# Kernel optimization log

Measured on AMD Instinct MI355X. Metric: run time of the kernel, lower is better.

Reference implementation:

```python
import jax, jax.numpy as jnp
import numpy as np

TEMPERATURE = 0.07
HARD_NEG_RATIO = 0.5
B, D, N_CLASSES = 2048, 512, 100


def setup_inputs() -> dict:
    key = jax.random.key(0)
    kf, kl = jax.random.split(key)
    features = jax.random.normal(kf, (B, D), dtype=jnp.float32)
    # L2-normalize as is standard for SupCon embeddings (keeps logits well-scaled)
    features = features / jnp.linalg.norm(features, axis=1, keepdims=True)
    labels = jax.random.randint(kl, (B,), 0, N_CLASSES, dtype=jnp.int64)
    return {"features": features, "labels": labels}


def reference(features, labels):
    b = features.shape[0]
    dt = features.dtype
    lab = labels.reshape(-1, 1)
    mask = (lab == lab.T).astype(dt)                       # [B,B] positives (incl. self)
    adc = (features @ features.T) / TEMPERATURE            # [B,B] logits
    logits_max = jax.lax.stop_gradient(jnp.max(adc, axis=1, keepdims=True))
    logits = adc - logits_max                              # row-stabilized
    logits_mask = 1.0 - jnp.eye(b, dtype=dt)               # exclude self
    negative_mask = (1.0 - mask) * logits_mask
    neg_b = negative_mask > 0

    # top-k hard-negative threshold: k-th largest negative logit (global over all pairs).
    # k is data-dependent, so use a full descending sort + dynamic gather (jit-safe).
    flat = jnp.where(neg_b, logits, -jnp.inf).ravel()      # [B*B]
    sorted_desc = -jnp.sort(-flat)
    n_neg = jnp.sum(neg_b)
    k = jnp.maximum(1, (HARD_NEG_RATIO * n_neg).astype(jnp.int32))  # floor, >=1
    threshold = sorted_desc[k - 1]
    hard_negatives_mask = ((logits >= threshold) & neg_b).astype(dt)

    final_mask = jnp.minimum(mask + hard_negatives_mask, 1.0) * logits_mask
    row_pos = final_mask.sum(axis=1)
    single_samples = (row_pos == 0).astype(dt)

    exp_logits = jnp.exp(logits) * logits_mask
    log_prob = logits - jnp.log(exp_logits.sum(axis=1, keepdims=True) + 1e-12)
    mean_log_prob_pos = (final_mask * log_prob).sum(axis=1) / (row_pos + single_samples)
    loss_vec = -mean_log_prob_pos * (1.0 - single_samples)
    loss = loss_vec.sum() / (b - single_samples.sum())
    return (loss, hard_negatives_mask, final_mask)
```

## Files before the change

kernel.cpp:

```cpp
#include <hip/hip_runtime.h>
#include <cstddef>

constexpr int Bn   = 2048;
constexpr int Dn   = 512;
constexpr int NCLS = 100;
constexpr int CAP  = 131072;
constexpr unsigned WWIN = 32768;


struct Ctl {
  unsigned above;
  unsigned candCount;
  unsigned singles;
  unsigned done;
  float    thrF;
  unsigned pad1;
  double   lossSum;
  unsigned hist[4096];
  unsigned cand[CAP];
};
static_assert(offsetof(Ctl, cand) % 16 == 0, "cand must be 16B aligned");
static_assert(offsetof(Ctl, cand) == 16416, "zeroed head size");

__device__ inline unsigned key_of(float L) {
  unsigned u = __float_as_uint(L);
  return (u & 0x80000000u) ? ~u : (u | 0x80000000u);
}
__device__ inline float key_to_float(unsigned key) {
  unsigned u = (key & 0x80000000u) ? (key ^ 0x80000000u) : ~key;
  return __uint_as_float(u);
}
__device__ inline unsigned wlo_key() {
  const float c0 = -1.0f / 0.07f;
  return key_of(c0) - (WWIN / 2);
}
__device__ inline void store16_a4(float* p, float4 v) {
  __builtin_memcpy((void*)p, &v, 16);
}

__global__ __launch_bounds__(256) void rowdot_k(const float* __restrict__ F,
                                                float* __restrict__ rm, Ctl* c) {
  const int i = blockIdx.x * 256 + threadIdx.x;
  const float4* p = (const float4*)(F + (size_t)i * Dn);
  float acc = 0.0f;
#pragma unroll 16
  for (int q = 0; q < 128; ++q) {
    const float4 f = p[q];
    acc = __builtin_fmaf(f.x, f.x, acc);
    acc = __builtin_fmaf(f.y, f.y, acc);
    acc = __builtin_fmaf(f.z, f.z, acc);
    acc = __builtin_fmaf(f.w, f.w, acc);
  }
  rm[i] = acc / 0.07f;
  unsigned* cz = (unsigned*)c;
  for (int idx = i; idx < 4104; idx += 2048) cz[idx] = 0;
}

__global__ __launch_bounds__(256) void gemm_adc(const float* __restrict__ F,
                                                const float* __restrict__ rm,
                                                const int* __restrict__ labels,
                                                float* __restrict__ adc, Ctl* c) {
  __shared__ float smem[4352];
  __shared__ int slabi[64], slabj[64];
  __shared__ float rmiA[64], rmjA[64];
  __shared__ unsigned wlist[1024];
  __shared__ unsigned wcnt, abcnt, gbase;
  const int t = threadIdx.x;
  int r = 0;
  { const int idx = blockIdx.x; while ((r + 1) * (r + 2) / 2 <= idx) ++r; }
  const int cc = blockIdx.x - r * (r + 1) / 2;
  const int i0 = r * 64, j0 = cc * 64;

  const int tx = t & 15, ty = t >> 4;
  const int lrow = t >> 2, lq = t & 3;

  if (t < 64) {
    slabi[t] = labels[i0 + t]; rmiA[t] = rm[i0 + t];
    slabj[t] = labels[j0 + t]; rmjA[t] = rm[j0 + t];
  }
  if (t == 0) { wcnt = 0; abcnt = 0; gbase = 0; }

  float acc[4][4] = {};
  const float* Ab = F + (size_t)(i0 + lrow) * Dn;
  const float* Bb = F + (size_t)(j0 + lrow) * Dn;
  float* As = smem;
  float* Bs = smem + 2176;

  float4 a = *(const float4*)(Ab + lq * 4);
  float4 b = *(const float4*)(Bb + lq * 4);
  {
    const int k0 = lq * 4;
    As[(k0 + 0) * 68 + lrow] = a.x; As[(k0 + 1) * 68 + lrow] = a.y;
    As[(k0 + 2) * 68 + lrow] = a.z; As[(k0 + 3) * 68 + lrow] = a.w;
    Bs[(k0 + 0) * 68 + lrow] = b.x; Bs[(k0 + 1) * 68 + lrow] = b.y;
    Bs[(k0 + 2) * 68 + lrow] = b.z; Bs[(k0 + 3) * 68 + lrow] = b.w;
  }
  __syncthreads();

  for (int ch = 0; ch < 32; ++ch) {
    const int cur = ch & 1, nxt = cur ^ 1;
    if (ch < 31) {
      const int kg = (ch + 1) * 16;
      a = *(const float4*)(Ab + kg + lq * 4);
      b = *(const float4*)(Bb + kg + lq * 4);
    }
    const float* Ac = As + cur * 1088;
    const float* Bc = Bs + cur * 1088;
#pragma unroll
    for (int k = 0; k < 16; ++k) {
      const float4 av = *(const float4*)(Ac + k * 68 + ty * 4);
      const float4 bv = *(const float4*)(Bc + k * 68 + tx * 4);
      const float aa[4] = {av.x, av.y, av.z, av.w};
      const float bb[4] = {bv.x, bv.y, bv.z, bv.w};
#pragma unroll
      for (int m = 0; m < 4; ++m)
#pragma unroll
        for (int n = 0; n < 4; ++n)
          acc[m][n] = __builtin_fmaf(aa[m], bb[n], acc[m][n]);
    }
    if (ch < 31) {
      const int k0 = lq * 4;
      float* An = As + nxt * 1088;
      float* Bm = Bs + nxt * 1088;
      An[(k0 + 0) * 68 + lrow] = a.x; An[(k0 + 1) * 68 + lrow] = a.y;
      An[(k0 + 2) * 68 + lrow] = a.z; An[(k0 + 3) * 68 + lrow] = a.w;
      Bm[(k0 + 0) * 68 + lrow] = b.x; Bm[(k0 + 1) * 68 + lrow] = b.y;
      Bm[(k0 + 2) * 68 + lrow] = b.z; Bm[(k0 + 3) * 68 + lrow] = b.w;
    }
    __syncthreads();
  }

  float v[4][4];
#pragma unroll
  for (int m = 0; m < 4; ++m) {
#pragma unroll
    for (int n = 0; n < 4; ++n) v[m][n] = acc[m][n] / 0.07f;
    float4 q = {v[m][0], v[m][1], v[m][2], v[m][3]};
    *(float4*)&adc[(size_t)(i0 + ty * 4 + m) * Bn + j0 + tx * 4] = q;
  }
  if (r != cc) {
    __syncthreads();
    float* T = smem;
#pragma unroll
    for (int m = 0; m < 4; ++m)
#pragma unroll
      for (int n = 0; n < 4; ++n)
        T[(tx * 4 + n) * 68 + (ty * 4 + m)] = v[m][n];
    __syncthreads();
#pragma unroll
    for (int e = 0; e < 4; ++e) {
      const int row2 = e * 16 + ty;
      *(float4*)&adc[(size_t)(j0 + row2) * Bn + i0 + tx * 4] =
          *(const float4*)(T + row2 * 68 + tx * 4);
    }
  }

  __syncthreads();
  const unsigned klo = wlo_key(), khi = klo + WWIN;
  unsigned myab = 0;
#pragma unroll
  for (int m = 0; m < 4; ++m) {
    const int gi = i0 + ty * 4 + m;
    const int li = slabi[ty * 4 + m];
    const float rmi = rmiA[ty * 4 + m];
#pragma unroll
    for (int n = 0; n < 4; ++n) {
      const int gj = j0 + tx * 4 + n;
      if (gi == gj || li == slabj[tx * 4 + n]) continue;
      const unsigned key = key_of(v[m][n] - rmi);
      if (key >= khi) ++myab;
      else if (key >= klo) {
        atomicAdd(&c->hist[(key - klo) >> 3], 1u);
        const unsigned p = atomicAdd(&wcnt, 1u);
        if (p < 1024u) wlist[p] = key;
      }
      if (r != cc) {
        const unsigned key2 = key_of(v[m][n] - rmjA[tx * 4 + n]);
        if (key2 >= khi) ++myab;
        else if (key2 >= klo) {
          atomicAdd(&c->hist[(key2 - klo) >> 3], 1u);
          const unsigned p = atomicAdd(&wcnt, 1u);
          if (p < 1024u) wlist[p] = key2;
        }
      }
    }
  }
  if (myab) atomicAdd(&abcnt, myab);
  __syncthreads();
  if (t == 0) {
    if (abcnt) atomicAdd(&c->above, abcnt);
    const unsigned nl = wcnt < 1024u ? wcnt : 1024u;
    gbase = nl ? atomicAdd(&c->candCount, nl) : 0u;
  }
  __syncthreads();
  const unsigned nl = wcnt < 1024u ? wcnt : 1024u;
  for (unsigned q = t; q < nl; q += 256) {
    const unsigned p = gbase + q;
    if (p < (unsigned)CAP) c->cand[p] = wlist[q];
  }
}

__global__ __launch_bounds__(256) void select_k(const int* __restrict__ labels, Ctl* c) {
  __shared__ unsigned cnt[NCLS];
  __shared__ unsigned tsum[256], suffix[256];
  __shared__ unsigned skk;
  __shared__ int sbd;
  __shared__ unsigned sab, m;
  __shared__ unsigned list[256];
  const int t = threadIdx.x;
  if (t < NCLS) cnt[t] = 0;
  if (t == 0) { m = 0; sbd = 0; sab = 0; }
  __syncthreads();
  for (int j = t; j < Bn; j += 256) atomicAdd(&cnt[labels[j]], 1u);
  __syncthreads();
  if (t == 0) {
    unsigned s = 0;
    for (int h = 0; h < NCLS; ++h) s += cnt[h] * cnt[h];
    unsigned nneg = (unsigned)Bn * Bn - s;
    unsigned k = nneg >> 1;
    if (k < 1) k = 1;
    skk = k;
  }
  const uint4* hp = (const uint4*)c->hist;
  uint4 h0 = hp[t * 4 + 0], h1 = hp[t * 4 + 1], h2 = hp[t * 4 + 2], h3 = hp[t * 4 + 3];
  const unsigned hv[16] = {h0.x, h0.y, h0.z, h0.w, h1.x, h1.y, h1.z, h1.w,
                           h2.x, h2.y, h2.z, h2.w, h3.x, h3.y, h3.z, h3.w};
  unsigned s = 0;
#pragma unroll
  for (int u = 0; u < 16; ++u) s += hv[u];
  tsum[t] = s;
  __syncthreads();
  if (t == 0) {
    unsigned acc = c->above;
    for (int q = 255; q >= 0; --q) { suffix[q] = acc; acc += tsum[q]; }
  }
  __syncthreads();
  const unsigned kk = skk;
  unsigned cum = suffix[t];
#pragma unroll
  for (int u = 15; u >= 0; --u) {
    if (cum < kk && cum + hv[u] >= kk) { sbd = t * 16 + u; sab = cum; }
    cum += hv[u];
  }
  __syncthreads();
  const int bd = sbd;
  const unsigned rr = kk - sab;
  const unsigned klo = wlo_key();
  unsigned n = c->candCount; if (n > (unsigned)CAP) n = (unsigned)CAP;
  const unsigned n4 = n >> 2;
  const uint4* cp = (const uint4*)c->cand;
  unsigned q = t;
  for (; q + 7u * 256u < n4; q += 8u * 256u) {
    uint4 v[8];
#pragma unroll
    for (int u = 0; u < 8; ++u) v[u] = cp[q + (unsigned)u * 256u];
#pragma unroll
    for (int u = 0; u < 8; ++u) {
      const unsigned ks[4] = {v[u].x, v[u].y, v[u].z, v[u].w};
#pragma unroll
      for (int w = 0; w < 4; ++w) {
        const unsigned d = ks[w] - klo;
        if (d < WWIN && (int)(d >> 3) == bd) {
          const unsigned p = atomicAdd(&m, 1u);
          if (p < 256u) list[p] = ks[w];
        }
      }
    }
  }
  for (; q < n4; q += 256u) {
    const uint4 v = cp[q];
    const unsigned ks[4] = {v.x, v.y, v.z, v.w};
#pragma unroll
    for (int w = 0; w < 4; ++w) {
      const unsigned d = ks[w] - klo;
      if (d < WWIN && (int)(d >> 3) == bd) {
        const unsigned p = atomicAdd(&m, 1u);
        if (p < 256u) list[p] = ks[w];
      }
    }
  }
  for (unsigned e = n4 * 4u + t; e < n; e += 256u) {
    const unsigned key = c->cand[e];
    const unsigned d = key - klo;
    if (d < WWIN && (int)(d >> 3) == bd) {
      const unsigned p = atomicAdd(&m, 1u);
      if (p < 256u) list[p] = key;
    }
  }
  __syncthreads();
  const unsigned mm = m > 256u ? 256u : m;
  for (unsigned e = t; e < mm; e += 256) {
    const unsigned v = list[e];
    unsigned g = 0, ge = 0;
    for (unsigned j = 0; j < mm; ++j) {
      g  += (list[j] > v);
      ge += (list[j] >= v);
    }
    if (g < rr && rr <= ge) c->thrF = key_to_float(v);
  }
}

__global__ __launch_bounds__(256) void final_k(const float* __restrict__ adc,
                                               const int* __restrict__ labels,
                                               const Ctl* __restrict__ c,
                                               float* __restrict__ out,
                                               double* __restrict__ lsum_g,
                                               unsigned* __restrict__ scnt_g) {
  __shared__ int slab[Bn];
  __shared__ double lsum[4];
  __shared__ unsigned sflag[4];
  const int t = threadIdx.x;
  const int lane = t & 63, w = t >> 6;
#pragma unroll
  for (int e = 0; e < 2; ++e)
    ((int4*)slab)[t + 256 * e] = ((const int4*)labels)[t + 256 * e];
  __syncthreads();
  const float thr = c->thrF;
  float* __restrict__ ohnm = out + 1;
  float* __restrict__ ofin = out + 1 + (size_t)Bn * Bn;

  const int i = blockIdx.x * 4 + w;
  const int li = slab[i];
  const float rm = adc[(size_t)i * Bn + i];
  const float4* rowp = (const float4*)(adc + (size_t)i * Bn);
  float se = 0.0f, sp = 0.0f;
  int pc = 0;
#pragma unroll
  for (int q = 0; q < 8; ++q) {
    const int j4 = lane + 64 * q;
    const float4 vv = rowp[j4];
    const int jb = j4 * 4;
    const float vs[4] = {vv.x, vv.y, vv.z, vv.w};
    float qh[4], qf[4];
#pragma unroll
    for (int u = 0; u < 4; ++u) {
      const int j = jb + u;
      const float L = vs[u] - rm;
      const bool offd = (j != i);
      const bool same = (slab[j] == li);
      const bool hnm  = offd && !same && (L >= thr);
      const bool fin  = offd && (same || hnm);
      if (offd) se += __expf(L);
      if (fin)  { sp += L; ++pc; }
      qh[u] = hnm ? 1.0f : 0.0f;
      qf[u] = fin ? 1.0f : 0.0f;
    }
    float4 h4 = {qh[0], qh[1], qh[2], qh[3]};
    float4 f4 = {qf[0], qf[1], qf[2], qf[3]};
    store16_a4(&ohnm[(size_t)i * Bn + jb], h4);
    store16_a4(&ofin[(size_t)i * Bn + jb], f4);
  }
  float pcf = (float)pc;
#pragma unroll
  for (int o = 32; o > 0; o >>= 1) {
    se  += __shfl_down(se,  o, 64);
    sp  += __shfl_down(sp,  o, 64);
    pcf += __shfl_down(pcf, o, 64);
  }
  if (lane == 0) {
    const double P = (double)pcf;
    const bool single = (P == 0.0);
    const double mlpp = ((double)sp - P * log((double)se + 1e-12)) / (P + (single ? 1.0 : 0.0));
    lsum[w]  = single ? 0.0 : -mlpp;
    sflag[w] = single ? 1u : 0u;
  }
  __syncthreads();
  if (t == 0) {
    lsum_g[blockIdx.x] = lsum[0] + lsum[1] + lsum[2] + lsum[3];
    scnt_g[blockIdx.x] = sflag[0] + sflag[1] + sflag[2] + sflag[3];
  }
}

__global__ __launch_bounds__(256) void finalize_k(const double* __restrict__ lsum_g,
                                                  const unsigned* __restrict__ scnt_g,
                                                  float* __restrict__ out) {
  __shared__ double wls[4];
  __shared__ unsigned wsc[4];
  const int t = threadIdx.x;
  const int lane = t & 63, w = t >> 6;
  double ls = lsum_g[t] + lsum_g[t + 256];
  unsigned sc = scnt_g[t] + scnt_g[t + 256];
#pragma unroll
  for (int o = 32; o > 0; o >>= 1) {
    ls += __shfl_down(ls, o, 64);
    sc += __shfl_down(sc, o, 64);
  }
  if (lane == 0) { wls[w] = ls; wsc[w] = sc; }
  __syncthreads();
  if (t == 0) {
    const double tot = wls[0] + wls[1] + wls[2] + wls[3];
    const unsigned sg = wsc[0] + wsc[1] + wsc[2] + wsc[3];
    out[0] = (float)(tot / ((double)Bn - (double)sg));
  }
}

extern "C" void kernel_launch(void* const* d_in, const int* in_sizes, int n_in,
                              void* d_out, int out_size, void* d_ws, size_t ws_size,
                              hipStream_t stream) {
  const float* F      = (const float*)d_in[0];
  const int*   labels = (const int*)d_in[1];
  float* out = (float*)d_out;

  char* ws = (char*)d_ws;
  Ctl*     c      = (Ctl*)ws;
  float*   rm     = (float*)(ws + 786432);
  double*  lsum_g = (double*)(ws + 802816);
  unsigned* scnt_g = (unsigned*)(ws + 806912);
  float*   adc    = (float*)(ws + (1u << 20));

  rowdot_k<<<Bn / 256, 256, 0, stream>>>(F, rm, c);
  gemm_adc<<<528, 256, 0, stream>>>(F, rm, labels, adc, c);
  select_k<<<1, 256, 0, stream>>>(labels, c);
  final_k<<<512, 256, 0, stream>>>(adc, labels, c, out, lsum_g, scnt_g);
  finalize_k<<<1, 256, 0, stream>>>(lsum_g, scnt_g, out);
}
```

Before: 173.6 us.

## Fold select and finalize kernels into predecessors via last-block counters

The single-block threshold selection is moved into the tail of the GEMM kernel, and the scalar loss reduction into the tail of the final kernel. In each case the last block to finish, found with an atomic completion counter, does the work. Cross-block data is read through agent-scope atomic loads after fences. This removes two kernel launches and their dependency gaps, at the cost of scalar rather than vectorized candidate loads and extra atomics and fences in every block. The rowdot kernel is also relaunched as 32 blocks of 64 threads.

```diff
diff --git a/kernel.cpp b/kernel.cpp
--- a/kernel.cpp
+++ b/kernel.cpp
@@ -37,10 +37,22 @@
 __device__ inline void store16_a4(float* p, float4 v) {
   __builtin_memcpy((void*)p, &v, 16);
 }
-
-__global__ __launch_bounds__(256) void rowdot_k(const float* __restrict__ F,
-                                                float* __restrict__ rm, Ctl* c) {
-  const int i = blockIdx.x * 256 + threadIdx.x;
+__device__ inline unsigned agent_load_u32(const unsigned* p) {
+  return __hip_atomic_load(p, __ATOMIC_RELAXED, __HIP_MEMORY_SCOPE_AGENT);
+}
+__device__ inline double agent_load_f64(const double* p) {
+  return __hip_atomic_load(p, __ATOMIC_RELAXED, __HIP_MEMORY_SCOPE_AGENT);
+}
+__device__ inline void agent_store_f64(double* p, double v) {
+  __hip_atomic_store(p, v, __ATOMIC_RELAXED, __HIP_MEMORY_SCOPE_AGENT);
+}
+__device__ inline void agent_store_u32(unsigned* p, unsigned v) {
+  __hip_atomic_store(p, v, __ATOMIC_RELAXED, __HIP_MEMORY_SCOPE_AGENT);
+}
+
+__global__ __launch_bounds__(64) void rowdot_k(const float* __restrict__ F,
+                                               float* __restrict__ rm, Ctl* c) {
+  const int i = blockIdx.x * 64 + threadIdx.x;
   const float4* p = (const float4*)(F + (size_t)i * Dn);
   float acc = 0.0f;
 #pragma unroll 16
@@ -65,6 +77,9 @@
   __shared__ float rmiA[64], rmjA[64];
   __shared__ unsigned wlist[1024];
   __shared__ unsigned wcnt, abcnt, gbase;
+  __shared__ unsigned amlast;
+  __shared__ unsigned skk2, sab2, m2;
+  __shared__ int sbd2;
   const int t = threadIdx.x;
   int r = 0;
   { const int idx = blockIdx.x; while ((r + 1) * (r + 2) / 2 <= idx) ++r; }
@@ -198,117 +213,104 @@
     const unsigned p = gbase + q;
     if (p < (unsigned)CAP) c->cand[p] = wlist[q];
   }
-}
-
-__global__ __launch_bounds__(256) void select_k(const int* __restrict__ labels, Ctl* c) {
-  __shared__ unsigned cnt[NCLS];
-  __shared__ unsigned tsum[256], suffix[256];
-  __shared__ unsigned skk;
-  __shared__ int sbd;
-  __shared__ unsigned sab, m;
-  __shared__ unsigned list[256];
-  const int t = threadIdx.x;
-  if (t < NCLS) cnt[t] = 0;
-  if (t == 0) { m = 0; sbd = 0; sab = 0; }
-  __syncthreads();
-  for (int j = t; j < Bn; j += 256) atomicAdd(&cnt[labels[j]], 1u);
-  __syncthreads();
-  if (t == 0) {
-    unsigned s = 0;
-    for (int h = 0; h < NCLS; ++h) s += cnt[h] * cnt[h];
-    unsigned nneg = (unsigned)Bn * Bn - s;
+
+  __syncthreads();
+  if (t == 0) {
+    __threadfence();
+    amlast = (atomicAdd(&c->done, 1u) == 527u) ? 1u : 0u;
+  }
+  __syncthreads();
+  if (!amlast) return;
+  __threadfence();
+
+  unsigned* s_cnt    = (unsigned*)smem;
+  unsigned* s_tsum   = (unsigned*)smem + 128;
+  unsigned* s_suffix = (unsigned*)smem + 384;
+  unsigned* s_list   = (unsigned*)smem + 640;
+  if (t < NCLS) s_cnt[t] = 0;
+  if (t == 0) { m2 = 0; sbd2 = 0; sab2 = 0; }
+  __syncthreads();
+  for (int j = t; j < Bn; j += 256) atomicAdd(&s_cnt[labels[j]], 1u);
+  __syncthreads();
+  if (t == 0) {
+    unsigned s2 = 0;
+    for (int hh = 0; hh < NCLS; ++hh) s2 += s_cnt[hh] * s_cnt[hh];
+    unsigned nneg = (unsigned)Bn * Bn - s2;
     unsigned k = nneg >> 1;
     if (k < 1) k = 1;
-    skk = k;
-  }
-  const uint4* hp = (const uint4*)c->hist;
-  uint4 h0 = hp[t * 4 + 0], h1 = hp[t * 4 + 1], h2 = hp[t * 4 + 2], h3 = hp[t * 4 + 3];
-  const unsigned hv[16] = {h0.x, h0.y, h0.z, h0.w, h1.x, h1.y, h1.z, h1.w,
-                           h2.x, h2.y, h2.z, h2.w, h3.x, h3.y, h3.z, h3.w};
-  unsigned s = 0;
-#pragma unroll
-  for (int u = 0; u < 16; ++u) s += hv[u];
-  tsum[t] = s;
-  __syncthreads();
-  if (t == 0) {
-    unsigned acc = c->above;
-    for (int q = 255; q >= 0; --q) { suffix[q] = acc; acc += tsum[q]; }
-  }
-  __syncthreads();
-  const unsigned kk = skk;
-  unsigned cum = suffix[t];
+    skk2 = k;
+  }
+  unsigned hv[16];
+  unsigned ssum = 0;
+#pragma unroll
+  for (int u = 0; u < 16; ++u) {
+    hv[u] = agent_load_u32(&c->hist[t * 16 + u]);
+    ssum += hv[u];
+  }
+  s_tsum[t] = ssum;
+  __syncthreads();
+  if (t == 0) {
+    unsigned accu = agent_load_u32(&c->above);
+    for (int q2 = 255; q2 >= 0; --q2) { s_suffix[q2] = accu; accu += s_tsum[q2]; }
+  }
+  __syncthreads();
+  const unsigned kk = skk2;
+  unsigned cum = s_suffix[t];
 #pragma unroll
   for (int u = 15; u >= 0; --u) {
-    if (cum < kk && cum + hv[u] >= kk) { sbd = t * 16 + u; sab = cum; }
+    if (cum < kk && cum + hv[u] >= kk) { sbd2 = t * 16 + u; sab2 = cum; }
     cum += hv[u];
   }
   __syncthreads();
-  const int bd = sbd;
-  const unsigned rr = kk - sab;
-  const unsigned klo = wlo_key();
-  unsigned n = c->candCount; if (n > (unsigned)CAP) n = (unsigned)CAP;
-  const unsigned n4 = n >> 2;
-  const uint4* cp = (const uint4*)c->cand;
-  unsigned q = t;
-  for (; q + 7u * 256u < n4; q += 8u * 256u) {
-    uint4 v[8];
-#pragma unroll
-    for (int u = 0; u < 8; ++u) v[u] = cp[q + (unsigned)u * 256u];
+  const int bd = sbd2;
+  const unsigned rrk = kk - sab2;
+  unsigned n = agent_load_u32(&c->candCount);
+  if (n > (unsigned)CAP) n = (unsigned)CAP;
+  unsigned e = t;
+  for (; e + 7u * 256u < n; e += 8u * 256u) {
+    unsigned ks[8];
+#pragma unroll
+    for (int u = 0; u < 8; ++u) ks[u] = agent_load_u32(&c->cand[e + (unsigned)u * 256u]);
 #pragma unroll
     for (int u = 0; u < 8; ++u) {
-      const unsigned ks[4] = {v[u].x, v[u].y, v[u].z, v[u].w};
-#pragma unroll
-      for (int w = 0; w < 4; ++w) {
-        const unsigned d = ks[w] - klo;
-        if (d < WWIN && (int)(d >> 3) == bd) {
-          const unsigned p = atomicAdd(&m, 1u);
-          if (p < 256u) list[p] = ks[w];
-        }
+      const unsigned d = ks[u] - klo;
+      if (d < WWIN && (int)(d >> 3) == bd) {
+        const unsigned p = atomicAdd(&m2, 1u);
+        if (p < 256u) s_list[p] = ks[u];
       }
     }
   }
-  for (; q < n4; q += 256u) {
-    const uint4 v = cp[q];
-    const unsigned ks[4] = {v.x, v.y, v.z, v.w};
-#pragma unroll
-    for (int w = 0; w < 4; ++w) {
-      const unsigned d = ks[w] - klo;
-      if (d < WWIN && (int)(d >> 3) == bd) {
-        const unsigned p = atomicAdd(&m, 1u);
-        if (p < 256u) list[p] = ks[w];
-      }
-    }
-  }
-  for (unsigned e = n4 * 4u + t; e < n; e += 256u) {
-    const unsigned key = c->cand[e];
-    const unsigned d = key - klo;
+  for (; e < n; e += 256u) {
+    const unsigned kv = agent_load_u32(&c->cand[e]);
+    const unsigned d = kv - klo;
     if (d < WWIN && (int)(d >> 3) == bd) {
-      const unsigned p = atomicAdd(&m, 1u);
-      if (p < 256u) list[p] = key;
-    }
-  }
-  __syncthreads();
-  const unsigned mm = m > 256u ? 256u : m;
-  for (unsigned e = t; e < mm; e += 256) {
-    const unsigned v = list[e];
+      const unsigned p = atomicAdd(&m2, 1u);
+      if (p < 256u) s_list[p] = kv;
+    }
+  }
+  __syncthreads();
+  const unsigned mm = m2 > 256u ? 256u : m2;
+  for (unsigned e2 = t; e2 < mm; e2 += 256) {
+    const unsigned vv2 = s_list[e2];
     unsigned g = 0, ge = 0;
-    for (unsigned j = 0; j < mm; ++j) {
-      g  += (list[j] > v);
-      ge += (list[j] >= v);
-    }
-    if (g < rr && rr <= ge) c->thrF = key_to_float(v);
+    for (unsigned j2 = 0; j2 < mm; ++j2) {
+      g  += (s_list[j2] > vv2);
+      ge += (s_list[j2] >= vv2);
+    }
+    if (g < rrk && rrk <= ge) c->thrF = key_to_float(vv2);
   }
 }
 
 __global__ __launch_bounds__(256) void final_k(const float* __restrict__ adc,
                                                const int* __restrict__ labels,
-                                               const Ctl* __restrict__ c,
+                                               Ctl* c,
                                                float* __restrict__ out,
                                                double* __restrict__ lsum_g,
                                                unsigned* __restrict__ scnt_g) {
   __shared__ int slab[Bn];
   __shared__ double lsum[4];
   __shared__ unsigned sflag[4];
+  __shared__ unsigned amlast;
   const int t = threadIdx.x;
   const int lane = t & 63, w = t >> 6;
 #pragma unroll
@@ -366,30 +368,27 @@
   }
   __syncthreads();
   if (t == 0) {
-    lsum_g[blockIdx.x] = lsum[0] + lsum[1] + lsum[2] + lsum[3];
-    scnt_g[blockIdx.x] = sflag[0] + sflag[1] + sflag[2] + sflag[3];
-  }
-}
-
-__global__ __launch_bounds__(256) void finalize_k(const double* __restrict__ lsum_g,
-                                                  const unsigned* __restrict__ scnt_g,
-                                                  float* __restrict__ out) {
-  __shared__ double wls[4];
-  __shared__ unsigned wsc[4];
-  const int t = threadIdx.x;
-  const int lane = t & 63, w = t >> 6;
-  double ls = lsum_g[t] + lsum_g[t + 256];
-  unsigned sc = scnt_g[t] + scnt_g[t + 256];
+    agent_store_f64(&lsum_g[blockIdx.x], lsum[0] + lsum[1] + lsum[2] + lsum[3]);
+    agent_store_u32(&scnt_g[blockIdx.x], sflag[0] + sflag[1] + sflag[2] + sflag[3]);
+    __threadfence();
+    amlast = (atomicAdd(&c->singles, 1u) == 511u) ? 1u : 0u;
+  }
+  __syncthreads();
+  if (!amlast) return;
+  __threadfence();
+
+  double ls = agent_load_f64(&lsum_g[t]) + agent_load_f64(&lsum_g[t + 256]);
+  unsigned sc = agent_load_u32(&scnt_g[t]) + agent_load_u32(&scnt_g[t + 256]);
 #pragma unroll
   for (int o = 32; o > 0; o >>= 1) {
     ls += __shfl_down(ls, o, 64);
     sc += __shfl_down(sc, o, 64);
   }
-  if (lane == 0) { wls[w] = ls; wsc[w] = sc; }
-  __syncthreads();
-  if (t == 0) {
-    const double tot = wls[0] + wls[1] + wls[2] + wls[3];
-    const unsigned sg = wsc[0] + wsc[1] + wsc[2] + wsc[3];
+  if (lane == 0) { lsum[w] = ls; sflag[w] = sc; }
+  __syncthreads();
+  if (t == 0) {
+    const double tot = lsum[0] + lsum[1] + lsum[2] + lsum[3];
+    const unsigned sg = sflag[0] + sflag[1] + sflag[2] + sflag[3];
     out[0] = (float)(tot / ((double)Bn - (double)sg));
   }
 }
@@ -402,15 +401,13 @@
   float* out = (float*)d_out;
 
   char* ws = (char*)d_ws;
-  Ctl*     c      = (Ctl*)ws;
-  float*   rm     = (float*)(ws + 786432);
-  double*  lsum_g = (double*)(ws + 802816);
+  Ctl*      c      = (Ctl*)ws;
+  float*    rm     = (float*)(ws + 786432);
+  double*   lsum_g = (double*)(ws + 802816);
   unsigned* scnt_g = (unsigned*)(ws + 806912);
-  float*   adc    = (float*)(ws + (1u << 20));
-
-  rowdot_k<<<Bn / 256, 256, 0, stream>>>(F, rm, c);
+  float*    adc    = (float*)(ws + (1u << 20));
+
+  rowdot_k<<<32, 64, 0, stream>>>(F, rm, c);
   gemm_adc<<<528, 256, 0, stream>>>(F, rm, labels, adc, c);
-  select_k<<<1, 256, 0, stream>>>(labels, c);
   final_k<<<512, 256, 0, stream>>>(adc, labels, c, out, lsum_g, scnt_g);
-  finalize_k<<<1, 256, 0, stream>>>(lsum_g, scnt_g, out);
-}
+}
```

Result: slower. 196.0 us (+12.9%).
